# Kernel optimization log

Measured on AMD Instinct MI355X. Metric: run time of the kernel, lower is better.

Reference implementation:

```python
import jax, jax.numpy as jnp
import numpy as np
from jax import lax

NUM_EMBEDDING = 512
D_EMBEDDING = 256
COMMITMENT_COST = 0.25
B = 131072


def setup_inputs() -> dict:
    key = jax.random.key(0)
    k1, k2, k3 = jax.random.split(key, 3)
    node_type = jax.random.randint(k1, (B,), 0, 10, dtype=jnp.int64 if jax.config.jax_enable_x64 else jnp.int32)
    node_representation = jax.random.normal(k2, (B, D_EMBEDDING), dtype=jnp.float32)
    # nn.Embedding default init: N(0, 1)
    codebook = jax.random.normal(k3, (NUM_EMBEDDING, D_EMBEDDING), dtype=jnp.float32)
    return {"node_type": node_type, "node_representation": node_representation, "codebook": codebook}


def _code_indices(node_type, z, codebook):
    # Map atom type -> codebook quadrant: C(5)->0, N(6)->1, O(7)->2, others->3
    K = codebook.shape[0]
    qsize = K // 4
    group = jnp.where(node_type == 5, 0,
            jnp.where(node_type == 6, 1,
            jnp.where(node_type == 7, 2, 3)))  # [b]
    # Squared L2 distances to all codes: ||z||^2 + ||e||^2 - 2 z.e  -> [b, K]
    d2 = (jnp.sum(z * z, axis=1, keepdims=True)
          + jnp.sum(codebook * codebook, axis=1)
          - 2.0 * (z @ codebook.T))
    col_group = jnp.arange(K) // qsize  # [K], quadrant of each code
    valid = group[:, None] == col_group[None, :]  # [b, K]
    # Masked argmin == per-quadrant argmin (+ quadrant offset), as in the original.
    return jnp.argmin(jnp.where(valid, d2, jnp.inf), axis=1)


def reference(node_type, node_representation, codebook):
    z = node_representation
    idx = _code_indices(node_type, z, codebook)          # [b]
    quantized = codebook[idx]                            # [b, d]
    vq_loss = jnp.mean((quantized - lax.stop_gradient(z)) ** 2)
    commitment_loss = COMMITMENT_COST * jnp.mean((z - lax.stop_gradient(quantized)) ** 2)
    # Straight-through estimator
    quantized_st = z + lax.stop_gradient(quantized - z)
    return (vq_loss, commitment_loss, idx, quantized_st)
```

## Files before the change

kernel.cpp:

```cpp
#include <hip/hip_runtime.h>


#define B_ROWS   131072
#define D_EMB    256
#define TPB      256
#define MAXT     8196
#define SGRID2   1025
#define THETA    0.0625f

#define WS_WSUM   0
#define WS_I64N   512
#define WS_GCNT   516
#define WS_GPOS   532
#define WS_NT     548
#define WS_CBH    1024
#define WS_CBL    (WS_CBH + 262144)
#define WS_EN     (WS_CBL + 262144)
#define WS_ROWS   (WS_EN + 2048)
#define WS_TD     (WS_ROWS + 524288)
#define WS_NEED_NEW (WS_TD + 4 * MAXT)
#define WS_FLAGS  8

typedef __attribute__((ext_vector_type(8))) short bf16x8;
typedef __attribute__((ext_vector_type(4))) float f32x4;

__device__ __forceinline__ float bf2f(unsigned short u) {
    return __uint_as_float(((unsigned)u) << 16);
}

__device__ __forceinline__ void splitA(const float4& a0, const float4& a1,
                                       bf16x8& ah, bf16x8& al) {
    float ff[8] = {a0.x, a0.y, a0.z, a0.w, a1.x, a1.y, a1.z, a1.w};
    #pragma unroll
    for (int j = 0; j < 8; ++j) {
        unsigned u = __float_as_uint(ff[j]);
        ah[j] = (short)(u >> 16);
        float r = ff[j] - __uint_as_float(u & 0xffff0000u);
        al[j] = (short)(__float_as_uint(r) >> 16);
    }
}

__global__ void vq_prep(const float* __restrict__ cbf, const int* __restrict__ nt,
                        unsigned short* __restrict__ cbh, unsigned short* __restrict__ cbl,
                        float* __restrict__ eN, int* __restrict__ flagI64) {
    const int code = blockIdx.x;
    const int lane = threadIdx.x;
    float4 v = *(const float4*)(cbf + code * 256 + lane * 4);

    unsigned u0 = __float_as_uint(v.x), u1 = __float_as_uint(v.y);
    unsigned u2 = __float_as_uint(v.z), u3 = __float_as_uint(v.w);
    ushort4 h = make_ushort4((unsigned short)(u0 >> 16), (unsigned short)(u1 >> 16),
                             (unsigned short)(u2 >> 16), (unsigned short)(u3 >> 16));
    float r0 = v.x - __uint_as_float(u0 & 0xffff0000u);
    float r1 = v.y - __uint_as_float(u1 & 0xffff0000u);
    float r2 = v.z - __uint_as_float(u2 & 0xffff0000u);
    float r3 = v.w - __uint_as_float(u3 & 0xffff0000u);
    ushort4 l = make_ushort4((unsigned short)(__float_as_uint(r0) >> 16),
                             (unsigned short)(__float_as_uint(r1) >> 16),
                             (unsigned short)(__float_as_uint(r2) >> 16),
                             (unsigned short)(__float_as_uint(r3) >> 16));
    *(ushort4*)(cbh + code * 256 + lane * 4) = h;
    *(ushort4*)(cbl + code * 256 + lane * 4) = l;

    float s = fmaf(v.x, v.x, fmaf(v.y, v.y, fmaf(v.z, v.z, v.w * v.w)));
    #pragma unroll
    for (int d = 1; d < 64; d <<= 1) s += __shfl_xor(s, d);
    if (lane == 0) eN[code] = s;

    if (code == 0) {
        int o = (nt[2 * lane + 1] != 0) ? 1 : 0;
        unsigned long long m = __ballot(o != 0);
        if (lane == 0) flagI64[0] = (m == 0ULL) ? 1 : 0;
    }
}

__global__ void vq_bin1(const int* __restrict__ nt, const int* __restrict__ fI,
                        int* __restrict__ gcnt) {
    __shared__ int c[4];
    const int tid = threadIdx.x;
    if (tid < 4) c[tid] = 0;
    __syncthreads();
    const int row = blockIdx.x * 256 + tid;
    const int t = fI[0] ? nt[2 * row] : nt[row];
    const int g = (t == 5) ? 0 : (t == 6) ? 1 : (t == 7) ? 2 : 3;
    atomicAdd(&c[g], 1);
    __syncthreads();
    if (tid < 4) atomicAdd(&gcnt[tid], c[tid]);
}

__global__ void vq_tiles32(const int* __restrict__ gcnt, int* __restrict__ gpos,
                           int* __restrict__ nT, int* __restrict__ td) {
    __shared__ int off[4], cnt[4], to[4], tot;
    if (threadIdx.x == 0) {
        int o = 0, t = 0;
        for (int g = 0; g < 4; ++g) {
            cnt[g] = gcnt[g];
            off[g] = o; o += cnt[g];
            int tc = (cnt[g] + 31) >> 5;
            to[g] = t; t += tc;
            gpos[g] = off[g];
        }
        tot = t; nT[0] = t;
    }
    __syncthreads();
    const int t = tot;
    for (int i = threadIdx.x; i < t; i += 64) {
        int g = 3;
        if (i < to[1]) g = 0; else if (i < to[2]) g = 1; else if (i < to[3]) g = 2;
        int b = i - to[g];
        int base = off[g] + b * 32;
        int nr = cnt[g] - b * 32; if (nr > 32) nr = 32;
        td[i] = nr | (base << 6) | (g << 23);
    }
}

__global__ void vq_bin2(const int* __restrict__ nt, const int* __restrict__ fI,
                        int* __restrict__ gpos, int* __restrict__ rows) {
    __shared__ int base[4], pos[4];
    const int tid = threadIdx.x;
    if (tid < 4) pos[tid] = 0;
    __syncthreads();
    const int row = blockIdx.x * 256 + tid;
    const int t = fI[0] ? nt[2 * row] : nt[row];
    const int g = (t == 5) ? 0 : (t == 6) ? 1 : (t == 7) ? 2 : 3;
    atomicAdd(&pos[g], 1);
    __syncthreads();
    if (tid < 4) { base[tid] = atomicAdd(&gpos[tid], pos[tid]); pos[tid] = 0; }
    __syncthreads();
    int p = atomicAdd(&pos[g], 1);
    rows[base[g] + p] = row;
}

__global__ __launch_bounds__(TPB, 3) void vq_score2(
    const float* __restrict__ zf,
    const float* __restrict__ cbf,
    const unsigned short* __restrict__ cbh,
    const unsigned short* __restrict__ cbl,
    const float* __restrict__ eN,
    const int* __restrict__ rows,
    const int* __restrict__ td,
    const int* __restrict__ nT,
    float* __restrict__ out,
    double* __restrict__ wsum)
{
    __shared__ int2   sT[4][16];
    __shared__ float2 sM[4][16];
    __shared__ float  sZZ[4][16];
    __shared__ double sRed[4];

    const int tid  = threadIdx.x;
    const int wave = tid >> 6;
    const int lane = tid & 63;
    const int col  = lane & 15;
    const int quad = lane >> 4;
    const int w    = blockIdx.x * 4 + wave;

    double lacc = 0.0;

    if (w < nT[0]) {
        const int d    = td[w];
        const int nr   = d & 63;
        const int base = (d >> 6) & 0x1FFFF;
        const int g    = d >> 23;
        const int nr0  = (nr < 16) ? nr : 16;
        const int nr1  = nr - 16;

        int ix0 = base + ((col < nr0) ? col : (nr0 - 1));
        int ix1 = (nr1 > 0) ? (base + 16 + ((col < nr1) ? col : (nr1 - 1))) : ix0;
        const int rowA0 = rows[ix0];
        const int rowA1 = rows[ix1];
        const float* za0 = zf + rowA0 * 256 + quad * 8;
        const float* za1 = zf + rowA1 * 256 + quad * 8;
        const unsigned short* bhp = cbh + (g * 128 + col) * 256 + quad * 8;
        const unsigned short* blp = cbl + (g * 128 + col) * 256 + quad * 8;

        f32x4 acc[2][8];
        #pragma unroll
        for (int st = 0; st < 2; ++st)
            #pragma unroll
            for (int t = 0; t < 8; ++t) acc[st][t] = (f32x4){0.f, 0.f, 0.f, 0.f};
        float zz0 = 0.f, zz1 = 0.f;

        #pragma unroll
        for (int c = 0; c < 8; ++c) {
            float4 a00 = *(const float4*)(za0 + c * 32);
            float4 a01 = *(const float4*)(za0 + c * 32 + 4);
            float4 a10 = *(const float4*)(za1 + c * 32);
            float4 a11 = *(const float4*)(za1 + c * 32 + 4);
            zz0 = fmaf(a00.x,a00.x,fmaf(a00.y,a00.y,fmaf(a00.z,a00.z,fmaf(a00.w,a00.w,zz0))));
            zz0 = fmaf(a01.x,a01.x,fmaf(a01.y,a01.y,fmaf(a01.z,a01.z,fmaf(a01.w,a01.w,zz0))));
            zz1 = fmaf(a10.x,a10.x,fmaf(a10.y,a10.y,fmaf(a10.z,a10.z,fmaf(a10.w,a10.w,zz1))));
            zz1 = fmaf(a11.x,a11.x,fmaf(a11.y,a11.y,fmaf(a11.z,a11.z,fmaf(a11.w,a11.w,zz1))));
            bf16x8 ah0, al0, ah1, al1;
            splitA(a00, a01, ah0, al0);
            splitA(a10, a11, ah1, al1);
            #pragma unroll
            for (int t = 0; t < 8; ++t) {
                bf16x8 bh = *(const bf16x8*)(bhp + t * 4096 + c * 32);
                bf16x8 bl = *(const bf16x8*)(blp + t * 4096 + c * 32);
                acc[0][t] = __builtin_amdgcn_mfma_f32_16x16x32_bf16(ah0, bh, acc[0][t], 0, 0, 0);
                acc[0][t] = __builtin_amdgcn_mfma_f32_16x16x32_bf16(al0, bh, acc[0][t], 0, 0, 0);
                acc[0][t] = __builtin_amdgcn_mfma_f32_16x16x32_bf16(ah0, bl, acc[0][t], 0, 0, 0);
                acc[1][t] = __builtin_amdgcn_mfma_f32_16x16x32_bf16(ah1, bh, acc[1][t], 0, 0, 0);
                acc[1][t] = __builtin_amdgcn_mfma_f32_16x16x32_bf16(al1, bh, acc[1][t], 0, 0, 0);
                acc[1][t] = __builtin_amdgcn_mfma_f32_16x16x32_bf16(ah1, bl, acc[1][t], 0, 0, 0);
            }
        }
        zz0 += __shfl_xor(zz0, 16); zz0 += __shfl_xor(zz0, 32);
        zz1 += __shfl_xor(zz1, 16); zz1 += __shfl_xor(zz1, 32);

        float e8[8];
        #pragma unroll
        for (int t = 0; t < 8; ++t) e8[t] = eN[g * 128 + t * 16 + col];

        for (int st = 0; st < 2; ++st) {
            const int nrs = st ? nr1 : nr0;
            if (nrs <= 0) continue;
            if (quad == 0) sZZ[wave][col] = st ? zz1 : zz0;

            #pragma unroll
            for (int r = 0; r < 4; ++r) {
                float m1 = __builtin_inff(), m2 = __builtin_inff();
                int   i1 = 0x7fffffff,      i2 = 0x7fffffff;
                #pragma unroll
                for (int t = 0; t < 8; ++t) {
                    float sc = e8[t] - 2.f * acc[st][t][r];
                    int   ci = t * 16 + col;
                    if (sc < m1 || (sc == m1 && ci < i1)) { m2 = m1; i2 = i1; m1 = sc; i1 = ci; }
                    else if (sc < m2 || (sc == m2 && ci < i2)) { m2 = sc; i2 = ci; }
                }
                #pragma unroll
                for (int d2 = 1; d2 < 16; d2 <<= 1) {
                    float b1 = __shfl_xor(m1, d2);
                    int  bi1 = __shfl_xor(i1, d2);
                    float b2 = __shfl_xor(m2, d2);
                    int  bi2 = __shfl_xor(i2, d2);
                    if (b1 < m1 || (b1 == m1 && bi1 < i1)) {
                        float om = m1; int oi = i1;
                        m1 = b1; i1 = bi1;
                        if (b2 < om || (b2 == om && bi2 < oi)) { m2 = b2; i2 = bi2; }
                        else                                   { m2 = om; i2 = oi; }
                    } else {
                        if (b1 < m2 || (b1 == m2 && bi1 < i2)) { m2 = b1; i2 = bi1; }
                    }
                }
                if (col == 0) {
                    sT[wave][quad * 4 + r] = make_int2(i1, i2);
                    sM[wave][quad * 4 + r] = make_float2(m1, m2);
                }
            }

            const int s  = lane >> 2;
            const int pq = lane & 3;
            const bool valid = (s < nrs);
            int grow = 0, c1 = 0, c2 = 0;
            float scm1 = 0.f, scm2 = 1e30f, zzr = 0.f;
            if (valid) {
                grow = rows[base + st * 16 + s];
                int2  tt = sT[wave][s];
                float2 mm = sM[wave][s];
                zzr = sZZ[wave][s];
                c1 = g * 128 + tt.x;
                c2 = g * 128 + tt.y;
                scm1 = mm.x; scm2 = mm.y;
            }
            int    wfin  = c1;
            double dfull = (double)(zzr + scm1);
            const bool need = valid && (scm2 - scm1 <= THETA);

            if (__any(need)) {
                double d1c = 0.0, d2c = 0.0;
                if (need) {
                    const float* zp = zf  + grow * 256 + pq * 64;
                    const float* p1 = cbf + c1 * 256 + pq * 64;
                    const float* p2 = cbf + c2 * 256 + pq * 64;
                    #pragma unroll 4
                    for (int it = 0; it < 16; ++it) {
                        float4 fz = *(const float4*)(zp + it * 4);
                        float4 g1 = *(const float4*)(p1 + it * 4);
                        float4 g2 = *(const float4*)(p2 + it * 4);
                        double e;
                        e = (double)fz.x - (double)g1.x; d1c = fma(e, e, d1c);
                        e = (double)fz.y - (double)g1.y; d1c = fma(e, e, d1c);
                        e = (double)fz.z - (double)g1.z; d1c = fma(e, e, d1c);
                        e = (double)fz.w - (double)g1.w; d1c = fma(e, e, d1c);
                        e = (double)fz.x - (double)g2.x; d2c = fma(e, e, d2c);
                        e = (double)fz.y - (double)g2.y; d2c = fma(e, e, d2c);
                        e = (double)fz.z - (double)g2.z; d2c = fma(e, e, d2c);
                        e = (double)fz.w - (double)g2.w; d2c = fma(e, e, d2c);
                    }
                }
                double t1 = d1c + __shfl_xor(d1c, 1); t1 += __shfl_xor(t1, 2);
                double t2 = d2c + __shfl_xor(d2c, 1); t2 += __shfl_xor(t2, 2);
                if (need) {
                    bool take1 = (t1 < t2) || (t1 == t2 && c1 < c2);
                    wfin  = take1 ? c1 : c2;
                    dfull = take1 ? t1 : t2;
                }
            }

            if (valid) {
                if (pq == 0) lacc += dfull;
                const float* pw = cbf + wfin * 256 + pq * 64;
                const int obase = 2 + B_ROWS + grow * 256 + pq * 64;
                float4 fprev = *(const float4*)(pw);
                *(float2*)(out + obase) = make_float2(fprev.x, fprev.y);
                #pragma unroll
                for (int it = 1; it < 16; ++it) {
                    float4 fcur = *(const float4*)(pw + it * 4);
                    *(float4*)(out + obase + (it - 1) * 4 + 2) =
                        make_float4(fprev.z, fprev.w, fcur.x, fcur.y);
                    fprev = fcur;
                }
                *(float2*)(out + obase + 62) = make_float2(fprev.z, fprev.w);
                if (pq == 0) out[2 + grow] = (float)wfin;
            }
        }
    }

    #pragma unroll
    for (int d2 = 1; d2 < 64; d2 <<= 1) lacc += __shfl_xor(lacc, d2);
    if (lane == 0) sRed[wave] = lacc;
    __syncthreads();
    if (tid == 0) atomicAdd(&wsum[blockIdx.x & 63], sRed[0] + sRed[1] + sRed[2] + sRed[3]);
}

__global__ void vq_detect(const unsigned short* cb, const int* nt, int* flag) {
    __shared__ int cnt, odd;
    if (threadIdx.x == 0) { cnt = 0; odd = 0; }
    __syncthreads();
    int c = 0, o = 0;
    for (int i = threadIdx.x; i < 512; i += 64) {
        unsigned short u = cb[2 * i];
        int e = (u >> 7) & 0xFF;
        if (e < 100 || e > 140) c++;
    }
    if (nt[2 * threadIdx.x + 1] != 0) o = 1;
    atomicAdd(&cnt, c);
    atomicAdd(&odd, o);
    __syncthreads();
    if (threadIdx.x == 0) {
        flag[0] = (cnt < 50) ? 1 : 0;
        flag[1] = (odd == 0) ? 1 : 0;
    }
}

__global__ __launch_bounds__(512, 2) void vq_main_f32(
    const int* __restrict__ nt,
    const float* __restrict__ zff,
    const float* __restrict__ cbf,
    float* __restrict__ out,
    double* __restrict__ wsum,
    const int* __restrict__ flag)
{
    if (flag[0] != 0) return;
    const int i64 = flag[1];

    __shared__ float  sE[256 * 132];
    __shared__ float  sZ[128 * 32];
    __shared__ int    sList[512];
    __shared__ int    sCnt[4], sPos[4];
    __shared__ int    sTop1[128], sTop2[128];
    __shared__ float  sEe[128];
    __shared__ double sRed[8];

    const int tid  = threadIdx.x;
    const int row0 = blockIdx.x * 512;

    if (tid < 4) { sCnt[tid] = 0; sPos[tid] = 0; }
    __syncthreads();
    {
        int t = i64 ? nt[2 * (row0 + tid)] : nt[row0 + tid];
        int g = (t == 5) ? 0 : (t == 6) ? 1 : (t == 7) ? 2 : 3;
        atomicAdd(&sCnt[g], 1);
        __syncthreads();
        int o1 = sCnt[0], o2 = o1 + sCnt[1], o3 = o2 + sCnt[2];
        int offg = (g == 0) ? 0 : (g == 1) ? o1 : (g == 2) ? o2 : o3;
        int p = atomicAdd(&sPos[g], 1);
        sList[offg + p] = row0 + tid;
    }
    __syncthreads();

    int cnt[4], off[4];
    cnt[0] = sCnt[0]; cnt[1] = sCnt[1]; cnt[2] = sCnt[2]; cnt[3] = sCnt[3];
    off[0] = 0; off[1] = cnt[0]; off[2] = off[1] + cnt[1]; off[3] = off[2] + cnt[2];

    const int ccol = tid & 31, rrow = tid >> 5;
    const int c0 = ccol * 4, rbase = rrow * 8;
    double lacc = 0.0;

    for (int gg = 0; gg < 4; ++gg) {
        const int n = cnt[gg];
        if (n == 0) continue;
        __syncthreads();
        for (int i = tid; i < 128 * 256; i += 512) {
            int c = i >> 8, k = i & 255;
            sE[k * 132 + c] = cbf[(gg * 128 + c) * 256 + k];
        }
        __syncthreads();
        if (tid < 128) {
            float s = 0.f;
            for (int k = 0; k < 256; ++k) { float v = sE[k * 132 + tid]; s = fmaf(v, v, s); }
            sEe[tid] = s;
        }
        __syncthreads();

        const int ntiles = (n + 127) >> 7;
        for (int tI = 0; tI < ntiles; ++tI) {
            const int tbase = off[gg] + tI * 128;
            const int nrows = min(128, n - tI * 128);
            float acc[8][4];
            #pragma unroll
            for (int r = 0; r < 8; ++r)
                #pragma unroll
                for (int q = 0; q < 4; ++q) acc[r][q] = 0.f;

            for (int kb = 0; kb < 8; ++kb) {
                __syncthreads();
                #pragma unroll
                for (int it = 0; it < 2; ++it) {
                    int i = it * 512 + tid;
                    int s = i >> 3, j = i & 7;
                    float4 v = make_float4(0.f, 0.f, 0.f, 0.f);
                    if (s < nrows) {
                        int gr = sList[tbase + s];
                        v = *(const float4*)(zff + gr * 256 + kb * 32 + j * 4);
                    }
                    *(float4*)&sZ[s * 32 + j * 4] = v;
                }
                __syncthreads();
                #pragma unroll
                for (int k4 = 0; k4 < 8; ++k4) {
                    const int kk = kb * 32 + k4 * 4;
                    const float4 e0 = *(const float4*)&sE[(kk + 0) * 132 + c0];
                    const float4 e1 = *(const float4*)&sE[(kk + 1) * 132 + c0];
                    const float4 e2 = *(const float4*)&sE[(kk + 2) * 132 + c0];
                    const float4 e3 = *(const float4*)&sE[(kk + 3) * 132 + c0];
                    #pragma unroll
                    for (int r = 0; r < 8; ++r) {
                        const float4 zv = *(const float4*)&sZ[(rbase + r) * 32 + k4 * 4];
                        acc[r][0] = fmaf(zv.x, e0.x, fmaf(zv.y, e1.x, fmaf(zv.z, e2.x, fmaf(zv.w, e3.x, acc[r][0]))));
                        acc[r][1] = fmaf(zv.x, e0.y, fmaf(zv.y, e1.y, fmaf(zv.z, e2.y, fmaf(zv.w, e3.y, acc[r][1]))));
                        acc[r][2] = fmaf(zv.x, e0.z, fmaf(zv.y, e1.z, fmaf(zv.z, e2.z, fmaf(zv.w, e3.z, acc[r][2]))));
                        acc[r][3] = fmaf(zv.x, e0.w, fmaf(zv.y, e1.w, fmaf(zv.z, e2.w, fmaf(zv.w, e3.w, acc[r][3]))));
                    }
                }
            }

            float eq[4] = { sEe[c0], sEe[c0 + 1], sEe[c0 + 2], sEe[c0 + 3] };
            for (int r = 0; r < 8; ++r) {
                float m1 = __builtin_inff(), m2 = __builtin_inff();
                int   i1 = 0x7fffffff,      i2 = 0x7fffffff;
                #pragma unroll
                for (int q = 0; q < 4; ++q) {
                    float sc = eq[q] - 2.f * acc[r][q];
                    int   ci = c0 + q;
                    if (sc < m1 || (sc == m1 && ci < i1)) { m2 = m1; i2 = i1; m1 = sc; i1 = ci; }
                    else if (sc < m2 || (sc == m2 && ci < i2)) { m2 = sc; i2 = ci; }
                }
                #pragma unroll
                for (int d = 1; d < 32; d <<= 1) {
                    float b1 = __shfl_xor(m1, d);
                    int  bi1 = __shfl_xor(i1, d);
                    float b2 = __shfl_xor(m2, d);
                    int  bi2 = __shfl_xor(i2, d);
                    if (b1 < m1 || (b1 == m1 && bi1 < i1)) {
                        float om = m1; int oi = i1;
                        m1 = b1; i1 = bi1;
                        if (b2 < om || (b2 == om && bi2 < oi)) { m2 = b2; i2 = bi2; }
                        else                                   { m2 = om; i2 = oi; }
                    } else {
                        if (b1 < m2 || (b1 == m2 && bi1 < i2)) { m2 = b1; i2 = bi1; }
                    }
                }
                if (ccol == 0) { sTop1[rbase + r] = i1; sTop2[rbase + r] = i2; }
            }
            __syncthreads();

            {
                const int s  = tid >> 2;
                const int pq = tid & 3;
                const bool valid = (s < nrows);
                double d1c = 0.0, d2c = 0.0;
                int gr = 0, c1g = 0, c2g = 0;
                if (valid) {
                    gr  = sList[tbase + s];
                    c1g = gg * 128 + sTop1[s];
                    c2g = gg * 128 + sTop2[s];
                    #pragma unroll 4
                    for (int it = 0; it < 16; ++it) {
                        float4 fz = *(const float4*)(zff + gr  * 256 + pq * 64 + it * 4);
                        float4 f1 = *(const float4*)(cbf + c1g * 256 + pq * 64 + it * 4);
                        float4 f2 = *(const float4*)(cbf + c2g * 256 + pq * 64 + it * 4);
                        double e;
                        e = (double)fz.x - (double)f1.x; d1c = fma(e, e, d1c);
                        e = (double)fz.y - (double)f1.y; d1c = fma(e, e, d1c);
                        e = (double)fz.z - (double)f1.z; d1c = fma(e, e, d1c);
                        e = (double)fz.w - (double)f1.w; d1c = fma(e, e, d1c);
                        e = (double)fz.x - (double)f2.x; d2c = fma(e, e, d2c);
                        e = (double)fz.y - (double)f2.y; d2c = fma(e, e, d2c);
                        e = (double)fz.z - (double)f2.z; d2c = fma(e, e, d2c);
                        e = (double)fz.w - (double)f2.w; d2c = fma(e, e, d2c);
                    }
                }
                double t1 = d1c + __shfl_xor(d1c, 1); t1 += __shfl_xor(t1, 2);
                double t2 = d2c + __shfl_xor(d2c, 1); t2 += __shfl_xor(t2, 2);
                if (valid) {
                    bool take1 = (t1 < t2) || (t1 == t2 && c1g < c2g);
                    int  w = take1 ? c1g : c2g;
                    lacc += take1 ? d1c : d2c;
                    const int obase = 2 + B_ROWS + gr * 256 + pq * 64;
                    #pragma unroll 4
                    for (int it = 0; it < 16; ++it) {
                        float4 f4 = *(const float4*)(cbf + w * 256 + pq * 64 + it * 4);
                        *(float2*)(out + obase + it * 4)     = make_float2(f4.x, f4.y);
                        *(float2*)(out + obase + it * 4 + 2) = make_float2(f4.z, f4.w);
                    }
                    if (pq == 0) out[2 + gr] = (float)w;
                }
            }
        }
    }

    #pragma unroll
    for (int d = 1; d < 64; d <<= 1) lacc += __shfl_xor(lacc, d);
    if ((tid & 63) == 0) sRed[tid >> 6] = lacc;
    __syncthreads();
    if (tid == 0) {
        double s = 0.0;
        #pragma unroll
        for (int i = 0; i < 8; ++i) s += sRed[i];
        atomicAdd(wsum, s);
    }
}

__global__ void vq_fin(const double* wsum, float* out, int n) {
    if (threadIdx.x == 0 && blockIdx.x == 0) {
        double m = 0.0;
        for (int i = 0; i < n; ++i) m += wsum[i];
        m /= ((double)B_ROWS * (double)D_EMB);
        out[0] = (float)m;
        out[1] = (float)(0.25 * m);
    }
}

extern "C" void kernel_launch(void* const* d_in, const int* in_sizes, int n_in,
                              void* d_out, int out_size, void* d_ws, size_t ws_size,
                              hipStream_t stream) {
    const int*   nt  = (const int*)d_in[0];
    const float* zf  = (const float*)d_in[1];
    const float* cbf = (const float*)d_in[2];
    float*  out  = (float*)d_out;
    double* wsum = (double*)((char*)d_ws + WS_WSUM);

    hipMemsetAsync(d_ws, 0, 1024, stream);

    if (ws_size >= (size_t)WS_NEED_NEW) {
        unsigned short* cbh  = (unsigned short*)((char*)d_ws + WS_CBH);
        unsigned short* cbl  = (unsigned short*)((char*)d_ws + WS_CBL);
        float* eN    = (float*)((char*)d_ws + WS_EN);
        int*   fI64  = (int*)((char*)d_ws + WS_I64N);
        int*   gcnt  = (int*)((char*)d_ws + WS_GCNT);
        int*   gpos  = (int*)((char*)d_ws + WS_GPOS);
        int*   nTp   = (int*)((char*)d_ws + WS_NT);
        int*   rowsp = (int*)((char*)d_ws + WS_ROWS);
        int*   tdp   = (int*)((char*)d_ws + WS_TD);
        vq_prep<<<512, 64, 0, stream>>>(cbf, nt, cbh, cbl, eN, fI64);
        vq_bin1<<<512, 256, 0, stream>>>(nt, fI64, gcnt);
        vq_tiles32<<<1, 64, 0, stream>>>(gcnt, gpos, nTp, tdp);
        vq_bin2<<<512, 256, 0, stream>>>(nt, fI64, gpos, rowsp);
        vq_score2<<<SGRID2, TPB, 0, stream>>>(zf, cbf, cbh, cbl, eN, rowsp, tdp, nTp,
                                              out, wsum);
        vq_fin<<<1, 64, 0, stream>>>(wsum, out, 64);
    } else {
        int* flag = (int*)((char*)d_ws + WS_FLAGS);
        vq_detect<<<1, 64, 0, stream>>>((const unsigned short*)cbf, nt, flag);
        vq_main_f32<<<256, 512, 0, stream>>>(nt, zf, cbf, out, wsum, flag);
        vq_fin<<<1, 64, 0, stream>>>(wsum, out, 1);
    }
}
```

Baseline: 420.5 us.

## Merge prep and binning kernels, compute tile descriptors inline, fuse final reduction

Cuts the launch chain from six kernels to three. Codebook splitting is merged with group counting, and the tile-descriptor kernel is removed so each score wave derives its tile from the group counts. The separate finalize kernel is replaced by a last-block-done reduction inside the score kernel. This targets per-launch overhead and serialization gaps between small kernels, at the cost of some redundant int64-detection work in each block and an extra atomic counter.

Result: slower. 505.5 us (+20.2%).

```diff
diff --git a/kernel.cpp b/kernel.cpp
--- a/kernel.cpp
+++ b/kernel.cpp
@@ -4,21 +4,18 @@
 #define B_ROWS   131072
 #define D_EMB    256
 #define TPB      256
-#define MAXT     8196
-#define SGRID2   1025
+#define SGRID    1025
 #define THETA    0.0625f
 
 #define WS_WSUM   0
-#define WS_I64N   512
+#define WS_DONE   512
 #define WS_GCNT   516
-#define WS_GPOS   532
-#define WS_NT     548
+#define WS_GPOSD  532
 #define WS_CBH    1024
 #define WS_CBL    (WS_CBH + 262144)
 #define WS_EN     (WS_CBL + 262144)
 #define WS_ROWS   (WS_EN + 2048)
-#define WS_TD     (WS_ROWS + 524288)
-#define WS_NEED_NEW (WS_TD + 4 * MAXT)
+#define WS_NEED   (WS_ROWS + 524288)
 #define WS_FLAGS  8
 
 typedef __attribute__((ext_vector_type(8))) short bf16x8;
@@ -40,113 +37,97 @@
     }
 }
 
-__global__ void vq_prep(const float* __restrict__ cbf, const int* __restrict__ nt,
-                        unsigned short* __restrict__ cbh, unsigned short* __restrict__ cbl,
-                        float* __restrict__ eN, int* __restrict__ flagI64) {
-    const int code = blockIdx.x;
-    const int lane = threadIdx.x;
-    float4 v = *(const float4*)(cbf + code * 256 + lane * 4);
-
-    unsigned u0 = __float_as_uint(v.x), u1 = __float_as_uint(v.y);
-    unsigned u2 = __float_as_uint(v.z), u3 = __float_as_uint(v.w);
-    ushort4 h = make_ushort4((unsigned short)(u0 >> 16), (unsigned short)(u1 >> 16),
-                             (unsigned short)(u2 >> 16), (unsigned short)(u3 >> 16));
-    float r0 = v.x - __uint_as_float(u0 & 0xffff0000u);
-    float r1 = v.y - __uint_as_float(u1 & 0xffff0000u);
-    float r2 = v.z - __uint_as_float(u2 & 0xffff0000u);
-    float r3 = v.w - __uint_as_float(u3 & 0xffff0000u);
-    ushort4 l = make_ushort4((unsigned short)(__float_as_uint(r0) >> 16),
-                             (unsigned short)(__float_as_uint(r1) >> 16),
-                             (unsigned short)(__float_as_uint(r2) >> 16),
-                             (unsigned short)(__float_as_uint(r3) >> 16));
-    *(ushort4*)(cbh + code * 256 + lane * 4) = h;
-    *(ushort4*)(cbl + code * 256 + lane * 4) = l;
-
-    float s = fmaf(v.x, v.x, fmaf(v.y, v.y, fmaf(v.z, v.z, v.w * v.w)));
-    #pragma unroll
-    for (int d = 1; d < 64; d <<= 1) s += __shfl_xor(s, d);
-    if (lane == 0) eN[code] = s;
-
-    if (code == 0) {
-        int o = (nt[2 * lane + 1] != 0) ? 1 : 0;
+__global__ void vq_prep2(const float* __restrict__ cbf, const int* __restrict__ nt,
+                         unsigned short* __restrict__ cbh, unsigned short* __restrict__ cbl,
+                         float* __restrict__ eN, int* __restrict__ gcnt) {
+    __shared__ int sI64, c4[4];
+    const int bid = blockIdx.x;
+    const int tid = threadIdx.x;
+
+    if (tid < 4) c4[tid] = 0;
+
+    if (tid < 64) {
+        const int lane = tid;
+        float4 v = *(const float4*)(cbf + bid * 256 + lane * 4);
+        unsigned u0 = __float_as_uint(v.x), u1 = __float_as_uint(v.y);
+        unsigned u2 = __float_as_uint(v.z), u3 = __float_as_uint(v.w);
+        ushort4 h = make_ushort4((unsigned short)(u0 >> 16), (unsigned short)(u1 >> 16),
+                                 (unsigned short)(u2 >> 16), (unsigned short)(u3 >> 16));
+        float r0 = v.x - __uint_as_float(u0 & 0xffff0000u);
+        float r1 = v.y - __uint_as_float(u1 & 0xffff0000u);
+        float r2 = v.z - __uint_as_float(u2 & 0xffff0000u);
+        float r3 = v.w - __uint_as_float(u3 & 0xffff0000u);
+        ushort4 l = make_ushort4((unsigned short)(__float_as_uint(r0) >> 16),
+                                 (unsigned short)(__float_as_uint(r1) >> 16),
+                                 (unsigned short)(__float_as_uint(r2) >> 16),
+                                 (unsigned short)(__float_as_uint(r3) >> 16));
+        *(ushort4*)(cbh + bid * 256 + lane * 4) = h;
+        *(ushort4*)(cbl + bid * 256 + lane * 4) = l;
+        float s = fmaf(v.x, v.x, fmaf(v.y, v.y, fmaf(v.z, v.z, v.w * v.w)));
+        #pragma unroll
+        for (int d = 1; d < 64; d <<= 1) s += __shfl_xor(s, d);
+        if (lane == 0) eN[bid] = s;
+    } else if (tid < 128) {
+        int o = (nt[2 * (tid - 64) + 1] != 0) ? 1 : 0;
         unsigned long long m = __ballot(o != 0);
-        if (lane == 0) flagI64[0] = (m == 0ULL) ? 1 : 0;
-    }
-}
-
-__global__ void vq_bin1(const int* __restrict__ nt, const int* __restrict__ fI,
-                        int* __restrict__ gcnt) {
-    __shared__ int c[4];
-    const int tid = threadIdx.x;
-    if (tid < 4) c[tid] = 0;
-    __syncthreads();
-    const int row = blockIdx.x * 256 + tid;
-    const int t = fI[0] ? nt[2 * row] : nt[row];
-    const int g = (t == 5) ? 0 : (t == 6) ? 1 : (t == 7) ? 2 : 3;
-    atomicAdd(&c[g], 1);
-    __syncthreads();
-    if (tid < 4) atomicAdd(&gcnt[tid], c[tid]);
-}
-
-__global__ void vq_tiles32(const int* __restrict__ gcnt, int* __restrict__ gpos,
-                           int* __restrict__ nT, int* __restrict__ td) {
-    __shared__ int off[4], cnt[4], to[4], tot;
-    if (threadIdx.x == 0) {
-        int o = 0, t = 0;
-        for (int g = 0; g < 4; ++g) {
-            cnt[g] = gcnt[g];
-            off[g] = o; o += cnt[g];
-            int tc = (cnt[g] + 31) >> 5;
-            to[g] = t; t += tc;
-            gpos[g] = off[g];
-        }
-        tot = t; nT[0] = t;
-    }
-    __syncthreads();
-    const int t = tot;
-    for (int i = threadIdx.x; i < t; i += 64) {
-        int g = 3;
-        if (i < to[1]) g = 0; else if (i < to[2]) g = 1; else if (i < to[3]) g = 2;
-        int b = i - to[g];
-        int base = off[g] + b * 32;
-        int nr = cnt[g] - b * 32; if (nr > 32) nr = 32;
-        td[i] = nr | (base << 6) | (g << 23);
-    }
-}
-
-__global__ void vq_bin2(const int* __restrict__ nt, const int* __restrict__ fI,
-                        int* __restrict__ gpos, int* __restrict__ rows) {
-    __shared__ int base[4], pos[4];
+        if (tid == 64) sI64 = (m == 0ULL) ? 1 : 0;
+    }
+    __syncthreads();
+
+    const int i64 = sI64;
+    const int row = bid * 256 + tid;
+    const int tv  = i64 ? nt[2 * row] : nt[row];
+    const int g   = (tv == 5) ? 0 : (tv == 6) ? 1 : (tv == 7) ? 2 : 3;
+    atomicAdd(&c4[g], 1);
+    __syncthreads();
+    if (tid < 4) atomicAdd(&gcnt[tid], c4[tid]);
+}
+
+__global__ void vq_binoff(const int* __restrict__ nt, const int* __restrict__ gcnt,
+                          int* __restrict__ gposD, int* __restrict__ rows) {
+    __shared__ int sI64, basev[4], pos[4];
     const int tid = threadIdx.x;
     if (tid < 4) pos[tid] = 0;
-    __syncthreads();
+    if (tid >= 64 && tid < 128) {
+        int o = (nt[2 * (tid - 64) + 1] != 0) ? 1 : 0;
+        unsigned long long m = __ballot(o != 0);
+        if (tid == 64) sI64 = (m == 0ULL) ? 1 : 0;
+    }
+    __syncthreads();
+    const int i64 = sI64;
     const int row = blockIdx.x * 256 + tid;
-    const int t = fI[0] ? nt[2 * row] : nt[row];
-    const int g = (t == 5) ? 0 : (t == 6) ? 1 : (t == 7) ? 2 : 3;
+    const int tv  = i64 ? nt[2 * row] : nt[row];
+    const int g   = (tv == 5) ? 0 : (tv == 6) ? 1 : (tv == 7) ? 2 : 3;
     atomicAdd(&pos[g], 1);
     __syncthreads();
-    if (tid < 4) { base[tid] = atomicAdd(&gpos[tid], pos[tid]); pos[tid] = 0; }
+    if (tid < 4) {
+        int c0 = gcnt[0], c1 = gcnt[1], c2 = gcnt[2];
+        int off = (tid == 0) ? 0 : (tid == 1) ? c0 : (tid == 2) ? (c0 + c1) : (c0 + c1 + c2);
+        basev[tid] = off + atomicAdd(&gposD[tid], pos[tid]);
+        pos[tid] = 0;
+    }
     __syncthreads();
     int p = atomicAdd(&pos[g], 1);
-    rows[base[g] + p] = row;
-}
-
-__global__ __launch_bounds__(TPB, 3) void vq_score2(
+    rows[basev[g] + p] = row;
+}
+
+__global__ __launch_bounds__(TPB, 3) void vq_score4(
     const float* __restrict__ zf,
     const float* __restrict__ cbf,
     const unsigned short* __restrict__ cbh,
     const unsigned short* __restrict__ cbl,
     const float* __restrict__ eN,
     const int* __restrict__ rows,
-    const int* __restrict__ td,
-    const int* __restrict__ nT,
+    const int* __restrict__ gcnt,
     float* __restrict__ out,
-    double* __restrict__ wsum)
+    double* __restrict__ wsum,
+    int* __restrict__ done)
 {
     __shared__ int2   sT[4][16];
     __shared__ float2 sM[4][16];
     __shared__ float  sZZ[4][16];
     __shared__ double sRed[4];
+    __shared__ int    sLast;
 
     const int tid  = threadIdx.x;
     const int wave = tid >> 6;
@@ -155,13 +136,22 @@
     const int quad = lane >> 4;
     const int w    = blockIdx.x * 4 + wave;
 
+    const int cnt0 = gcnt[0], cnt1 = gcnt[1], cnt2 = gcnt[2], cnt3 = gcnt[3];
+    const int off1 = cnt0, off2 = off1 + cnt1, off3 = off2 + cnt2;
+    const int tl0 = (cnt0 + 31) >> 5, tl1 = (cnt1 + 31) >> 5, tl2 = (cnt2 + 31) >> 5;
+    const int tl3 = (cnt3 + 31) >> 5;
+    const int to1 = tl0, to2 = to1 + tl1, to3 = to2 + tl2, tot = to3 + tl3;
+
     double lacc = 0.0;
 
-    if (w < nT[0]) {
-        const int d    = td[w];
-        const int nr   = d & 63;
-        const int base = (d >> 6) & 0x1FFFF;
-        const int g    = d >> 23;
+    if (w < tot) {
+        int g, b, offg, cntg;
+        if (w < to1)      { g = 0; b = w;       offg = 0;    cntg = cnt0; }
+        else if (w < to2) { g = 1; b = w - to1; offg = off1; cntg = cnt1; }
+        else if (w < to3) { g = 2; b = w - to2; offg = off2; cntg = cnt2; }
+        else              { g = 3; b = w - to3; offg = off3; cntg = cnt3; }
+        const int base = offg + b * 32;
+        int nr = cntg - b * 32; if (nr > 32) nr = 32;
         const int nr0  = (nr < 16) ? nr : 16;
         const int nr1  = nr - 16;
 
@@ -322,7 +312,22 @@
     for (int d2 = 1; d2 < 64; d2 <<= 1) lacc += __shfl_xor(lacc, d2);
     if (lane == 0) sRed[wave] = lacc;
     __syncthreads();
-    if (tid == 0) atomicAdd(&wsum[blockIdx.x & 63], sRed[0] + sRed[1] + sRed[2] + sRed[3]);
+    if (tid == 0) {
+        atomicAdd(&wsum[blockIdx.x & 63], sRed[0] + sRed[1] + sRed[2] + sRed[3]);
+        __threadfence();
+        sLast = (atomicAdd(done, 1) == (int)gridDim.x - 1) ? 1 : 0;
+    }
+    __syncthreads();
+    if (sLast && tid < 64) {
+        double v = atomicAdd(&wsum[tid], 0.0);
+        #pragma unroll
+        for (int d2 = 1; d2 < 64; d2 <<= 1) v += __shfl_xor(v, d2);
+        if (tid == 0) {
+            double m = v / ((double)B_ROWS * (double)D_EMB);
+            out[0] = (float)m;
+            out[1] = (float)(0.25 * m);
+        }
+    }
 }
 
 __global__ void vq_detect(const unsigned short* cb, const int* nt, int* flag) {
@@ -555,23 +560,18 @@
 
     hipMemsetAsync(d_ws, 0, 1024, stream);
 
-    if (ws_size >= (size_t)WS_NEED_NEW) {
+    if (ws_size >= (size_t)WS_NEED) {
         unsigned short* cbh  = (unsigned short*)((char*)d_ws + WS_CBH);
         unsigned short* cbl  = (unsigned short*)((char*)d_ws + WS_CBL);
         float* eN    = (float*)((char*)d_ws + WS_EN);
-        int*   fI64  = (int*)((char*)d_ws + WS_I64N);
         int*   gcnt  = (int*)((char*)d_ws + WS_GCNT);
-        int*   gpos  = (int*)((char*)d_ws + WS_GPOS);
-        int*   nTp   = (int*)((char*)d_ws + WS_NT);
+        int*   gposD = (int*)((char*)d_ws + WS_GPOSD);
+        int*   donep = (int*)((char*)d_ws + WS_DONE);
         int*   rowsp = (int*)((char*)d_ws + WS_ROWS);
-        int*   tdp   = (int*)((char*)d_ws + WS_TD);
-        vq_prep<<<512, 64, 0, stream>>>(cbf, nt, cbh, cbl, eN, fI64);
-        vq_bin1<<<512, 256, 0, stream>>>(nt, fI64, gcnt);
-        vq_tiles32<<<1, 64, 0, stream>>>(gcnt, gpos, nTp, tdp);
-        vq_bin2<<<512, 256, 0, stream>>>(nt, fI64, gpos, rowsp);
-        vq_score2<<<SGRID2, TPB, 0, stream>>>(zf, cbf, cbh, cbl, eN, rowsp, tdp, nTp,
-                                              out, wsum);
-        vq_fin<<<1, 64, 0, stream>>>(wsum, out, 64);
+        vq_prep2<<<512, 256, 0, stream>>>(cbf, nt, cbh, cbl, eN, gcnt);
+        vq_binoff<<<512, 256, 0, stream>>>(nt, gcnt, gposD, rowsp);
+        vq_score4<<<SGRID, TPB, 0, stream>>>(zf, cbf, cbh, cbl, eN, rowsp, gcnt,
+                                             out, wsum, donep);
     } else {
         int* flag = (int*)((char*)d_ws + WS_FLAGS);
         vq_detect<<<1, 64, 0, stream>>>((const unsigned short*)cbf, nt, flag);
```
